# Optimization experiments

Hardware: AMD Instinct MI355X
Metric: run time of the kernel (lower is better)

The kernel has to match this reference:

```python
import jax, jax.numpy as jnp
import numpy as np

N_NODES = 100000
N_EDGES = 640000
D_IN = 128
HIDDEN = 256
OUT = 256
NUM_GRAPHS = 256


def setup_inputs() -> dict:
    key = jax.random.key(0)
    ks = jax.random.split(key, 8)
    x = jax.random.normal(ks[0], (N_NODES, D_IN), dtype=jnp.float32)
    edge_index = jax.random.randint(ks[1], (2, N_EDGES), 0, N_NODES, dtype=jnp.int64)
    batch = jnp.sort(jax.random.randint(ks[2], (N_NODES,), 0, NUM_GRAPHS, dtype=jnp.int64))
    s1 = 1.0 / np.sqrt(D_IN)
    s2 = 1.0 / np.sqrt(HIDDEN)
    W1_l = jax.random.normal(ks[3], (D_IN, HIDDEN), dtype=jnp.float32) * s1
    W1_r = jax.random.normal(ks[4], (D_IN, HIDDEN), dtype=jnp.float32) * s1
    b1 = jnp.zeros((HIDDEN,), dtype=jnp.float32)
    W2_l = jax.random.normal(ks[5], (HIDDEN, OUT), dtype=jnp.float32) * s2
    W2_r = jax.random.normal(ks[6], (HIDDEN, OUT), dtype=jnp.float32) * s2
    b2 = jnp.zeros((OUT,), dtype=jnp.float32)
    return {"x": x, "edge_index": edge_index, "batch": batch,
            "W1_l": W1_l, "b1": b1, "W1_r": W1_r,
            "W2_l": W2_l, "b2": b2, "W2_r": W2_r}


def _sage_conv(x, src, dst, W_l, b_l, W_r):
    # PyG SAGEConv, aggr='mean': lin_l(mean_{j in N(i)} x_j) + lin_r(x_i)
    n = x.shape[0]
    msgs = x[src]                                              # [E, d] gather
    agg = jax.ops.segment_sum(msgs, dst, num_segments=n)       # [N, d] scatter-add
    cnt = jax.ops.segment_sum(jnp.ones((src.shape[0],), x.dtype), dst, num_segments=n)
    mean = agg / jnp.maximum(cnt, 1.0)[:, None]
    return mean @ W_l + b_l + x @ W_r


def reference(x, edge_index, batch, W1_l, b1, W1_r, W2_l, b2, W2_r):
    src, dst = edge_index[0], edge_index[1]
    h = jax.nn.relu(_sage_conv(x, src, dst, W1_l, b1, W1_r))
    h = _sage_conv(h, src, dst, W2_l, b2, W2_r)
    # global_add_pool: segment sum over per-node graph ids
    return jax.ops.segment_sum(h, batch, num_segments=NUM_GRAPHS)  # [G, OUT]
```

## Files before the change

kernel.cpp:

```cpp
#include <hip/hip_runtime.h>

#define NN 100000
#define NE 640000
#define DIN 128
#define DH 256
#define DOUT 256
#define NG 256
#define NB1 ((NN + 255) / 256)

#define PECH 157
#define CPE (4 * PECH)
#define PEB ((NE + CPE - 1) / CPE)
#define GSP 8

#define PNB 1024
#define CHN2 ((NN + PNB - 1) / PNB)

#define BCH 4096
#define BNB ((NE + BCH - 1) / BCH)

#define ANW 8
#define AGW ((NN + ANW - 1) / ANW)
#define AGB ((AGW + 3) / 4)

typedef __bf16 bf16_t;
typedef __bf16 bf16x8 __attribute__((ext_vector_type(8)));
typedef float f32x4 __attribute__((ext_vector_type(4)));
typedef float f32v2 __attribute__((ext_vector_type(2)));

#if __has_builtin(__builtin_amdgcn_cvt_pk_fp8_f32) && __has_builtin(__builtin_amdgcn_cvt_pk_f32_fp8)
#define USE_HW_FP8 1
#else
#define USE_HW_FP8 0
#endif

#if !USE_HW_FP8
__device__ __forceinline__ unsigned f32_to_fp8_1(float f) {
  unsigned sg = (__float_as_uint(f) >> 31) << 7;
  float af = fabsf(f);
  unsigned body;
  if (af < 0.015625f) {
    body = (unsigned)(int)rintf(af * 512.0f);
  } else {
    unsigned bits = __float_as_uint(af);
    unsigned rb = bits + 0x7FFFFu + ((bits >> 20) & 1u);
    unsigned e = rb >> 23;
    body = ((e - 120u) << 3) | ((rb >> 20) & 7u);
  }
  return (sg | body) & 0xffu;
}
__device__ __forceinline__ float fp8_to_f32_1(unsigned b) {
  unsigned s = b >> 7, e = (b >> 3) & 15u, m = b & 7u;
  float v = (e == 0) ? (float)m * 0.001953125f
                     : __uint_as_float(((e + 120u) << 23) | (m << 20));
  return s ? -v : v;
}
#endif

__device__ __forceinline__ unsigned pack4_fp8(float v0, float v1, float v2, float v3) {
#if USE_HW_FP8
  int u = __builtin_amdgcn_cvt_pk_fp8_f32(v0, v1, 0, false);
  u = __builtin_amdgcn_cvt_pk_fp8_f32(v2, v3, u, true);
  return (unsigned)u;
#else
  return f32_to_fp8_1(v0) | (f32_to_fp8_1(v1) << 8) |
         (f32_to_fp8_1(v2) << 16) | (f32_to_fp8_1(v3) << 24);
#endif
}

__device__ __forceinline__ unsigned short pack2_fp8(float v0, float v1) {
#if USE_HW_FP8
  int u = __builtin_amdgcn_cvt_pk_fp8_f32(v0, v1, 0, false);
  return (unsigned short)(u & 0xffff);
#else
  return (unsigned short)(f32_to_fp8_1(v0) | (f32_to_fp8_1(v1) << 8));
#endif
}

__device__ __forceinline__ void unpack4_fp8(unsigned v, float* o) {
#if USE_HW_FP8
  f32v2 a = __builtin_amdgcn_cvt_pk_f32_fp8((int)v, false);
  f32v2 b = __builtin_amdgcn_cvt_pk_f32_fp8((int)v, true);
  o[0] = a[0]; o[1] = a[1]; o[2] = b[0]; o[3] = b[1];
#else
  o[0] = fp8_to_f32_1(v & 0xffu);         o[1] = fp8_to_f32_1((v >> 8) & 0xffu);
  o[2] = fp8_to_f32_1((v >> 16) & 0xffu); o[3] = fp8_to_f32_1(v >> 24);
#endif
}

__device__ __forceinline__ void unpack8_fp8(uint2 v, float* o) {
  unpack4_fp8(v.x, o);
  unpack4_fp8(v.y, o + 4);
}

__device__ __forceinline__ void unpack2_fp8(unsigned v, float* o) {
#if USE_HW_FP8
  f32v2 a = __builtin_amdgcn_cvt_pk_f32_fp8((int)v, false);
  o[0] = a[0]; o[1] = a[1];
#else
  o[0] = fp8_to_f32_1(v & 0xffu); o[1] = fp8_to_f32_1((v >> 8) & 0xffu);
#endif
}

__global__ void k_xcast(const float* __restrict__ x, unsigned char* __restrict__ xf8) {
  size_t i = ((size_t)blockIdx.x * 256 + threadIdx.x) * 8;
  if (i >= (size_t)NN * DIN) return;
  float4 a = *(const float4*)(x + i), b = *(const float4*)(x + i + 4);
  uint2 p;
  p.x = pack4_fp8(a.x, a.y, a.z, a.w);
  p.y = pack4_fp8(b.x, b.y, b.z, b.w);
  *(uint2*)(xf8 + i) = p;
}

__global__ void k_count(const int* __restrict__ dst, int* __restrict__ cnt) {
  int e = blockIdx.x * 256 + threadIdx.x;
  if (e < NE) atomicAdd(&cnt[dst[e]], 1);
}

__global__ void k_scan1(const int* __restrict__ cnt, int* __restrict__ rowptr,
                        int* __restrict__ part) {
  __shared__ int s[256];
  int t = threadIdx.x, i = blockIdx.x * 256 + t;
  int v = (i < NN) ? cnt[i] : 0;
  s[t] = v; __syncthreads();
#pragma unroll
  for (int off = 1; off < 256; off <<= 1) {
    int u = (t >= off) ? s[t - off] : 0;
    __syncthreads();
    s[t] += u;
    __syncthreads();
  }
  if (i < NN) rowptr[i] = s[t] - v;
  if (t == 255) part[blockIdx.x] = s[255];
}

__global__ void k_scan2(int* __restrict__ part) {
  __shared__ int s[512];
  int t = threadIdx.x;
  int v = (t < NB1) ? part[t] : 0;
  s[t] = v; __syncthreads();
#pragma unroll
  for (int off = 1; off < 512; off <<= 1) {
    int u = (t >= off) ? s[t - off] : 0;
    __syncthreads();
    s[t] += u;
    __syncthreads();
  }
  if (t < NB1) part[t] = s[t] - v;
}

__global__ void k_scan3(int* __restrict__ rowptr, const int* __restrict__ part) {
  int i = blockIdx.x * 256 + threadIdx.x;
  if (i < NN) rowptr[i] += part[i >> 8];
  if (i == 0) rowptr[NN] = NE;
}

__global__ void k_gstart2(const int* __restrict__ batch, const int* __restrict__ rowptr,
                          int* __restrict__ gstart, unsigned* __restrict__ wg) {
  int n = blockIdx.x * 256 + threadIdx.x;
  if (n >= NN) return;
  int b = batch[n];
  int prev = (n == 0) ? -1 : batch[n - 1];
  for (int g = prev + 1; g <= b; ++g) gstart[g] = n;
  if (n == NN - 1) {
    for (int g = b + 1; g <= NG; ++g) gstart[g] = NN;
  }
  int e0 = rowptr[n], e1 = rowptr[n + 1];
  unsigned val = ((unsigned)b << 16) | (unsigned)(e1 - e0);
  for (int e = e0; e < e1; ++e) wg[e] = val;
}

__global__ void k_bucket(const int* __restrict__ src, const int* __restrict__ dst,
                         const int* __restrict__ rowptr, int* __restrict__ fill,
                         int* __restrict__ col) {
  int cls = blockIdx.x & 7;
  int cb = blockIdx.x >> 3;
  int e0 = cb * BCH;
  int e1 = (e0 + BCH < NE) ? e0 + BCH : NE;
  for (int e = e0 + threadIdx.x; e < e1; e += 256) {
    int d = dst[e];
    if (((d >> 4) & 7) == cls) {
      int p = rowptr[d] + atomicAdd(&fill[d], 1);
      col[p] = src[e];
    }
  }
}

__global__ void k_agg1(const int* __restrict__ rowptr, const int* __restrict__ col,
                       const unsigned char* __restrict__ xf8, unsigned char* __restrict__ ag1f8) {
  int wid = (blockIdx.x * 256 + threadIdx.x) >> 6;
  int lane = threadIdx.x & 63;
  int n0 = wid * ANW;
  if (n0 >= NN) return;
  int n1 = n0 + ANW; if (n1 > NN) n1 = NN;
  int e = rowptr[n0];
  int eTot = rowptr[n1];
  int n = n0;
  int estart = e;
  int eend = rowptr[n0 + 1];
  float a0 = 0.f, a1 = 0.f;
#define AFLUSH()                                                              \
  do {                                                                        \
    float r = (eend > estart) ? __builtin_amdgcn_rcpf((float)(eend - estart)) \
                              : 0.f;                                          \
    *(unsigned short*)(ag1f8 + (size_t)n * DIN + lane * 2) =                  \
        pack2_fp8(a0 * r, a1 * r);                                            \
    a0 = 0.f; a1 = 0.f;                                                       \
    estart = eend; n++;                                                       \
    if (n < n1) eend = rowptr[n + 1];                                         \
  } while (0)
  while (e + 8 <= eTot) {
    unsigned v[8];
#pragma unroll
    for (int i = 0; i < 8; ++i) {
      int s = col[e + i];
      v[i] = *(const unsigned short*)(xf8 + (size_t)s * DIN + lane * 2);
    }
#pragma unroll
    for (int i = 0; i < 8; ++i) {
      while (e + i >= eend) AFLUSH();
      float o[2];
      unpack2_fp8(v[i], o);
      a0 += o[0]; a1 += o[1];
    }
    e += 8;
  }
  while (e < eTot) {
    int s = col[e];
    unsigned v = *(const unsigned short*)(xf8 + (size_t)s * DIN + lane * 2);
    while (e >= eend) AFLUSH();
    float o[2];
    unpack2_fp8(v, o);
    a0 += o[0]; a1 += o[1];
    ++e;
  }
  while (n < n1) AFLUSH();
#undef AFLUSH
}

__global__ void k_pack1(const float* __restrict__ Wl, const float* __restrict__ Wr,
                        bf16_t* __restrict__ Bp) {
  int t = blockIdx.x * 256 + threadIdx.x;
  if (t >= 8192) return;
  int lane = t & 63, nt = (t >> 6) & 15, kc = t >> 10;
  int n = nt * 16 + (lane & 15);
  int k0 = kc * 32 + (lane >> 4) * 8;
  bf16_t* o = Bp + ((size_t)(kc * 16 + nt) * 64 + lane) * 8;
  for (int j = 0; j < 8; ++j) {
    int k = k0 + j;
    float v = (k < 128) ? Wl[k * 256 + n] : Wr[(k - 128) * 256 + n];
    o[j] = (bf16_t)v;
  }
}

__launch_bounds__(256, 4)
__global__ void k_gemm1(const unsigned char* __restrict__ xf8,
                        const unsigned char* __restrict__ ag1f8,
                        const float* __restrict__ b1,
                        const bf16_t* __restrict__ Bp, unsigned char* __restrict__ hf8) {
  __shared__ unsigned char smem[64 * 512];
  int n0 = blockIdx.x * 64;
  int tid = threadIdx.x;
  {
    int row = tid >> 2, part = tid & 3;
    int node = n0 + row;
    unsigned sw = (row & 7) << 4;
    const uint2* ap = (const uint2*)(ag1f8 + (size_t)node * DIN);
    const uint2* xp = (const uint2*)(xf8 + (size_t)node * DIN);
#pragma unroll
    for (int i = 0; i < 4; ++i) {
      int mi = i * 4 + part;
      uint2 va = {0u, 0u}, vx = {0u, 0u};
      if (node < NN) { va = ap[mi]; vx = xp[mi]; }
      float oa[8], ox[8];
      unpack8_fp8(va, oa);
      unpack8_fp8(vx, ox);
      bf16x8 wa, wx;
#pragma unroll
      for (int j = 0; j < 8; ++j) { wa[j] = (bf16_t)oa[j]; wx[j] = (bf16_t)ox[j]; }
      *(bf16x8*)(smem + row * 512 + (((unsigned)(mi * 16)) ^ sw)) = wa;
      *(bf16x8*)(smem + row * 512 + ((unsigned)(256 + mi * 16) ^ sw)) = wx;
    }
  }
  __syncthreads();
  int wave = tid >> 6, lane = tid & 63, lhi = lane >> 4, llo = lane & 15;
  f32x4 acc[4][4] = {};
  const bf16x8* bptr = (const bf16x8*)Bp;
#pragma unroll
  for (int kc = 0; kc < 8; ++kc) {
    bf16x8 a[4], b[4];
#pragma unroll
    for (int mi = 0; mi < 4; ++mi) {
      int row = mi * 16 + llo;
      unsigned cb = ((unsigned)((kc * 32 + lhi * 8) * 2)) ^ ((row & 7) << 4);
      a[mi] = *(const bf16x8*)(smem + row * 512 + cb);
    }
#pragma unroll
    for (int ni = 0; ni < 4; ++ni)
      b[ni] = bptr[(kc * 16 + wave * 4 + ni) * 64 + lane];
#pragma unroll
    for (int mi = 0; mi < 4; ++mi)
#pragma unroll
      for (int ni = 0; ni < 4; ++ni)
        acc[mi][ni] = __builtin_amdgcn_mfma_f32_16x16x32_bf16(a[mi], b[ni], acc[mi][ni], 0, 0, 0);
  }
  float bias[4];
#pragma unroll
  for (int ni = 0; ni < 4; ++ni) bias[ni] = b1[wave * 64 + ni * 16 + llo];
#pragma unroll
  for (int mi = 0; mi < 4; ++mi)
#pragma unroll
    for (int j = 0; j < 4; ++j) {
      int node = n0 + mi * 16 + lhi * 4 + j;
      if (node < NN) {
        float v0 = fmaxf(acc[mi][0][j] + bias[0], 0.f);
        float v1 = fmaxf(acc[mi][1][j] + bias[1], 0.f);
        float v2 = fmaxf(acc[mi][2][j] + bias[2], 0.f);
        float v3 = fmaxf(acc[mi][3][j] + bias[3], 0.f);
        unsigned u = pack4_fp8(v0, v1, v2, v3);
        *(unsigned*)(hf8 + (size_t)node * 256 + wave * 64 + llo * 4) = u;
      }
    }
}

__global__ void k_poolE2(const int* __restrict__ col, const unsigned* __restrict__ wg,
                         const unsigned char* __restrict__ hf8, float* __restrict__ Y1) {
  __shared__ float gbuf[GSP][256];
  int tid = threadIdx.x;
  int c0 = blockIdx.x * CPE;
  int c1 = (c0 + CPE < NE) ? c0 + CPE : NE;
  if (c0 >= c1) return;
  int gmin = (int)(wg[c0] >> 16), gmax = (int)(wg[c1 - 1] >> 16);
  bool ldsok = (gmax - gmin) < GSP;
  for (int i = tid; i < GSP * 256; i += 256) (&gbuf[0][0])[i] = 0.f;
  __syncthreads();
  int wv = tid >> 6, lane = tid & 63;
  int e0 = __builtin_amdgcn_readfirstlane(c0 + wv * PECH);
  int e1 = e0 + PECH; if (e1 > c1) e1 = c1;
  int dmb = ((lane >> 4) << 6) | (lane & 15);
  float acc[4] = {0.f, 0.f, 0.f, 0.f};
  int curg = -1;
#define EFLUSH() do { if (curg >= 0) {                                        \
    if (ldsok) { float* gp = gbuf[curg - gmin];                               \
      atomicAdd(gp + (dmb | 0),  acc[0]); atomicAdd(gp + (dmb | 16), acc[1]); \
      atomicAdd(gp + (dmb | 32), acc[2]); atomicAdd(gp + (dmb | 48), acc[3]); \
    } else { float* yp = Y1 + (size_t)curg * 256;                             \
      unsafeAtomicAdd(yp + (dmb | 0),  acc[0]);                               \
      unsafeAtomicAdd(yp + (dmb | 16), acc[1]);                               \
      unsafeAtomicAdd(yp + (dmb | 32), acc[2]);                               \
      unsafeAtomicAdd(yp + (dmb | 48), acc[3]); }                             \
    acc[0] = acc[1] = acc[2] = acc[3] = 0.f; } } while (0)
  if (e0 < e1) {
    int e = e0;
    for (; e + 16 <= e1; e += 16) {
      unsigned wvv[16]; unsigned hv[16];
#pragma unroll
      for (int i = 0; i < 16; ++i) {
        int c = col[e + i];
        wvv[i] = wg[e + i];
        hv[i] = *(const unsigned*)(hf8 + (size_t)c * 256 + lane * 4);
      }
#pragma unroll
      for (int i = 0; i < 16; ++i) {
        int g = (int)(wvv[i] >> 16);
        if (g != curg) { EFLUSH(); curg = g; }
        float w = __builtin_amdgcn_rcpf((float)(wvv[i] & 0xffffu));
        float o[4]; unpack4_fp8(hv[i], o);
        acc[0] += w * o[0]; acc[1] += w * o[1];
        acc[2] += w * o[2]; acc[3] += w * o[3];
      }
    }
    for (; e < e1; ++e) {
      int c = col[e]; unsigned wv2 = wg[e];
      unsigned hvv = *(const unsigned*)(hf8 + (size_t)c * 256 + lane * 4);
      int g = (int)(wv2 >> 16);
      if (g != curg) { EFLUSH(); curg = g; }
      float w = __builtin_amdgcn_rcpf((float)(wv2 & 0xffffu));
      float o[4]; unpack4_fp8(hvv, o);
      acc[0] += w * o[0]; acc[1] += w * o[1];
      acc[2] += w * o[2]; acc[3] += w * o[3];
    }
    EFLUSH();
  }
#undef EFLUSH
  __syncthreads();
  if (ldsok) {
    int ng = gmax - gmin + 1;
    for (int gi = 0; gi < ng; ++gi)
      unsafeAtomicAdd(&Y1[(size_t)(gmin + gi) * 256 + tid], gbuf[gi][tid]);
  }
}

__global__ void k_poolN(const int* __restrict__ batch, const unsigned char* __restrict__ hf8,
                        float* __restrict__ Y2) {
  __shared__ float gbuf[GSP][256];
  int tid = threadIdx.x;
  int n0 = blockIdx.x * CHN2;
  int n1 = (n0 + CHN2 < NN) ? n0 + CHN2 : NN;
  if (n0 >= n1) return;
  int gmin = batch[n0], gmax = batch[n1 - 1];
  bool ldsok = (gmax - gmin) < GSP;
  for (int i = tid; i < GSP * 256; i += 256) (&gbuf[0][0])[i] = 0.f;
  __syncthreads();
  int wv = tid >> 6, lane = tid & 63;
  const int per = (CHN2 + 3) >> 2;
  int a0 = n0 + wv * per;
  int a1 = a0 + per; if (a1 > n1) a1 = n1;
  int dmb = ((lane >> 4) << 6) | (lane & 15);
  float acc[4] = {0.f, 0.f, 0.f, 0.f};
  int curg = -1;
#define NFLUSH() do { if (curg >= 0) {                                        \
    if (ldsok) { float* gp = gbuf[curg - gmin];                               \
      atomicAdd(gp + (dmb | 0),  acc[0]); atomicAdd(gp + (dmb | 16), acc[1]); \
      atomicAdd(gp + (dmb | 32), acc[2]); atomicAdd(gp + (dmb | 48), acc[3]); \
    } else { float* yp = Y2 + (size_t)curg * 256;                             \
      unsafeAtomicAdd(yp + (dmb | 0),  acc[0]);                               \
      unsafeAtomicAdd(yp + (dmb | 16), acc[1]);                               \
      unsafeAtomicAdd(yp + (dmb | 32), acc[2]);                               \
      unsafeAtomicAdd(yp + (dmb | 48), acc[3]); }                             \
    acc[0] = acc[1] = acc[2] = acc[3] = 0.f; } } while (0)
  for (int n = a0; n < a1; ++n) {
    int g = batch[n];
    if (g != curg) { NFLUSH(); curg = g; }
    unsigned v = *(const unsigned*)(hf8 + (size_t)n * 256 + lane * 4);
    float o[4]; unpack4_fp8(v, o);
    acc[0] += o[0]; acc[1] += o[1]; acc[2] += o[2]; acc[3] += o[3];
  }
  NFLUSH();
#undef NFLUSH
  __syncthreads();
  if (ldsok) {
    int ng = gmax - gmin + 1;
    for (int gi = 0; gi < ng; ++gi)
      unsafeAtomicAdd(&Y2[(size_t)(gmin + gi) * 256 + tid], gbuf[gi][tid]);
  }
}

__global__ void k_out2(const float* __restrict__ Y1, const float* __restrict__ Y2,
                       const float* __restrict__ W2l, const float* __restrict__ W2r,
                       const float* __restrict__ b2, const int* __restrict__ gstart,
                       float* __restrict__ out) {
  __shared__ float ys[128];
  int g = blockIdx.x, ks = blockIdx.y, t = threadIdx.x;
  const float* Ysrc = (ks < 2) ? Y1 : Y2;
  const float* Wsrc = (ks < 2) ? W2l : W2r;
  int kbase = (ks & 1) * 128;
  if (t < 128) ys[t] = Ysrc[(size_t)g * 256 + kbase + t];
  __syncthreads();
  float s = 0.f;
  const float* wp = Wsrc + (size_t)kbase * 256 + t;
#pragma unroll 8
  for (int k = 0; k < 128; ++k) s += ys[k] * wp[(size_t)k * 256];
  if (ks == 0) {
    float cntf = (float)(gstart[g + 1] - gstart[g]);
    s += b2[t] * cntf;
  }
  unsafeAtomicAdd(&out[(size_t)g * 256 + t], s);
}

extern "C" void kernel_launch(void* const* d_in, const int* in_sizes, int n_in,
                              void* d_out, int out_size, void* d_ws, size_t ws_size,
                              hipStream_t stream) {
  const float* x   = (const float*)d_in[0];
  const int*   ei  = (const int*)d_in[1];
  const int*   bat = (const int*)d_in[2];
  const float* W1l = (const float*)d_in[3];
  const float* b1  = (const float*)d_in[4];
  const float* W1r = (const float*)d_in[5];
  const float* W2l = (const float*)d_in[6];
  const float* b2  = (const float*)d_in[7];
  const float* W2r = (const float*)d_in[8];
  const int* src = ei;
  const int* dst = ei + NE;

  char* ws = (char*)d_ws;
  size_t off = 0;
  int* cnt     = (int*)(ws + off); off += ((size_t)NN * 4 + 255) & ~(size_t)255;
  int* rowptr  = (int*)(ws + off); off += ((size_t)(NN + 1) * 4 + 255) & ~(size_t)255;
  int* part    = (int*)(ws + off); off += 512 * 4;
  int* fill    = (int*)(ws + off); off += ((size_t)NN * 4 + 255) & ~(size_t)255;
  int* gstart  = (int*)(ws + off); off += ((size_t)(NG + 1) * 4 + 255) & ~(size_t)255;
  int* col     = (int*)(ws + off); off += (size_t)NE * 4;
  unsigned* wg = (unsigned*)(ws + off); off += (size_t)NE * 4;
  bf16_t* Bp1  = (bf16_t*)(ws + off); off += (size_t)256 * 256 * 2;
  float* Y1    = (float*)(ws + off); off += (size_t)NG * 256 * 4;
  float* Y2    = (float*)(ws + off); off += (size_t)NG * 256 * 4;
  unsigned char* xf8 = (unsigned char*)(ws + off); off += (size_t)NN * DIN;
  unsigned char* ag1f8 = (unsigned char*)(ws + off); off += (size_t)NN * DIN;
  unsigned char* hf8 = (unsigned char*)(ws + off); off += (size_t)NN * DH;

  hipMemsetAsync(cnt, 0, (size_t)NN * 4, stream);
  hipMemsetAsync(fill, 0, (size_t)NN * 4, stream);
  hipMemsetAsync(Y1, 0, (size_t)NG * 256 * 4 * 2, stream);
  hipMemsetAsync(d_out, 0, (size_t)out_size * 4, stream);
  k_xcast<<<NN * DIN / 8 / 256, 256, 0, stream>>>(x, xf8);
  k_pack1<<<32, 256, 0, stream>>>(W1l, W1r, Bp1);
  k_count<<<(NE + 255) / 256, 256, 0, stream>>>(dst, cnt);
  k_scan1<<<NB1, 256, 0, stream>>>(cnt, rowptr, part);
  k_scan2<<<1, 512, 0, stream>>>(part);
  k_scan3<<<NB1, 256, 0, stream>>>(rowptr, part);
  k_gstart2<<<NB1, 256, 0, stream>>>(bat, rowptr, gstart, wg);
  k_bucket<<<BNB * 8, 256, 0, stream>>>(src, dst, rowptr, fill, col);
  k_agg1<<<AGB, 256, 0, stream>>>(rowptr, col, xf8, ag1f8);
  k_gemm1<<<(NN + 63) / 64, 256, 0, stream>>>(xf8, ag1f8, b1, Bp1, hf8);
  k_poolE2<<<PEB, 256, 0, stream>>>(col, wg, hf8, Y1);
  k_poolN<<<PNB, 256, 0, stream>>>(bat, hf8, Y2);
  k_out2<<<dim3(NG, 4), 256, 0, stream>>>(Y1, Y2, W2l, W2r, b2, gstart, (float*)d_out);
}
```

Before: 202.1 us.

## Fuse neighbor mean aggregation into GEMM1 and merge small setup and pool kernels

The first-layer neighbor aggregation now runs inside the GEMM kernel. Each wave gathers fp8 neighbor rows for 16 nodes and writes the bf16 means straight into shared memory, so the ag1f8 intermediate is no longer written to and read back from global memory. The x cast, edge count and weight pack kernels are merged into one launch, the scan fixup is folded into the gstart/wg kernel, and the two pooling kernels become one grid with block ranges. This removes several launches and a global round trip, but the irregular gather now sits inside the GEMM block, which may stall the MFMA work and lower its occupancy.

```diff
diff --git a/kernel.cpp b/kernel.cpp
--- a/kernel.cpp
+++ b/kernel.cpp
@@ -19,12 +19,12 @@
 #define BCH 4096
 #define BNB ((NE + BCH - 1) / BCH)
 
-#define ANW 8
-#define AGW ((NN + ANW - 1) / ANW)
-#define AGB ((AGW + 3) / 4)
+#define XCB (NN * DIN / 8 / 256)
+#define CTB ((NE + 255) / 256)
 
 typedef __bf16 bf16_t;
 typedef __bf16 bf16x8 __attribute__((ext_vector_type(8)));
+typedef __bf16 bf16x2 __attribute__((ext_vector_type(2)));
 typedef float f32x4 __attribute__((ext_vector_type(4)));
 typedef float f32v2 __attribute__((ext_vector_type(2)));
 
@@ -68,15 +68,6 @@
 #endif
 }
 
-__device__ __forceinline__ unsigned short pack2_fp8(float v0, float v1) {
-#if USE_HW_FP8
-  int u = __builtin_amdgcn_cvt_pk_fp8_f32(v0, v1, 0, false);
-  return (unsigned short)(u & 0xffff);
-#else
-  return (unsigned short)(f32_to_fp8_1(v0) | (f32_to_fp8_1(v1) << 8));
-#endif
-}
-
 __device__ __forceinline__ void unpack4_fp8(unsigned v, float* o) {
 #if USE_HW_FP8
   f32v2 a = __builtin_amdgcn_cvt_pk_f32_fp8((int)v, false);
@@ -88,11 +79,6 @@
 #endif
 }
 
-__device__ __forceinline__ void unpack8_fp8(uint2 v, float* o) {
-  unpack4_fp8(v.x, o);
-  unpack4_fp8(v.y, o + 4);
-}
-
 __device__ __forceinline__ void unpack2_fp8(unsigned v, float* o) {
 #if USE_HW_FP8
   f32v2 a = __builtin_amdgcn_cvt_pk_f32_fp8((int)v, false);
@@ -102,22 +88,38 @@
 #endif
 }
 
-__global__ void k_xcast(const float* __restrict__ x, unsigned char* __restrict__ xf8) {
-  size_t i = ((size_t)blockIdx.x * 256 + threadIdx.x) * 8;
-  if (i >= (size_t)NN * DIN) return;
-  float4 a = *(const float4*)(x + i), b = *(const float4*)(x + i + 4);
-  uint2 p;
-  p.x = pack4_fp8(a.x, a.y, a.z, a.w);
-  p.y = pack4_fp8(b.x, b.y, b.z, b.w);
-  *(uint2*)(xf8 + i) = p;
-}
-
-__global__ void k_count(const int* __restrict__ dst, int* __restrict__ cnt) {
-  int e = blockIdx.x * 256 + threadIdx.x;
-  if (e < NE) atomicAdd(&cnt[dst[e]], 1);
-}
-
-__global__ void k_scan1(const int* __restrict__ cnt, int* __restrict__ rowptr,
+__global__ void k_pre(const float* __restrict__ x, const int* __restrict__ dst,
+                      const float* __restrict__ Wl, const float* __restrict__ Wr,
+                      unsigned char* __restrict__ xf8, int* __restrict__ cnt,
+                      bf16_t* __restrict__ Bp) {
+  int b = blockIdx.x;
+  if (b < XCB) {
+    size_t i = ((size_t)b * 256 + threadIdx.x) * 8;
+    float4 a = *(const float4*)(x + i), c = *(const float4*)(x + i + 4);
+    uint2 p;
+    p.x = pack4_fp8(a.x, a.y, a.z, a.w);
+    p.y = pack4_fp8(c.x, c.y, c.z, c.w);
+    *(uint2*)(xf8 + i) = p;
+  } else if (b < XCB + CTB) {
+    int e = (b - XCB) * 256 + threadIdx.x;
+    if (e < NE) atomicAdd(&cnt[dst[e]], 1);
+  } else {
+    int t = (b - XCB - CTB) * 256 + threadIdx.x;
+    if (t < 8192) {
+      int lane = t & 63, nt = (t >> 6) & 15, kc = t >> 10;
+      int n = nt * 16 + (lane & 15);
+      int k0 = kc * 32 + (lane >> 4) * 8;
+      bf16_t* o = Bp + ((size_t)(kc * 16 + nt) * 64 + lane) * 8;
+      for (int j = 0; j < 8; ++j) {
+        int k = k0 + j;
+        float v = (k < 128) ? Wl[k * 256 + n] : Wr[(k - 128) * 256 + n];
+        o[j] = (bf16_t)v;
+      }
+    }
+  }
+}
+
+__global__ void k_scan1(const int* __restrict__ cnt, int* __restrict__ rpl,
                         int* __restrict__ part) {
   __shared__ int s[256];
   int t = threadIdx.x, i = blockIdx.x * 256 + t;
@@ -130,7 +132,7 @@
     s[t] += u;
     __syncthreads();
   }
-  if (i < NN) rowptr[i] = s[t] - v;
+  if (i < NN) rpl[i] = s[t] - v;
   if (t == 255) part[blockIdx.x] = s[255];
 }
 
@@ -149,25 +151,23 @@
   if (t < NB1) part[t] = s[t] - v;
 }
 
-__global__ void k_scan3(int* __restrict__ rowptr, const int* __restrict__ part) {
-  int i = blockIdx.x * 256 + threadIdx.x;
-  if (i < NN) rowptr[i] += part[i >> 8];
-  if (i == 0) rowptr[NN] = NE;
-}
-
-__global__ void k_gstart2(const int* __restrict__ batch, const int* __restrict__ rowptr,
-                          int* __restrict__ gstart, unsigned* __restrict__ wg) {
+__global__ void k_finish(const int* __restrict__ rpl, const int* __restrict__ part,
+                         const int* __restrict__ batch, int* __restrict__ rowptr,
+                         int* __restrict__ gstart, unsigned* __restrict__ wg) {
   int n = blockIdx.x * 256 + threadIdx.x;
   if (n >= NN) return;
+  int r0 = rpl[n] + part[n >> 8];
+  int r1 = (n + 1 < NN) ? (rpl[n + 1] + part[(n + 1) >> 8]) : NE;
+  rowptr[n] = r0;
+  if (n == 0) rowptr[NN] = NE;
   int b = batch[n];
   int prev = (n == 0) ? -1 : batch[n - 1];
   for (int g = prev + 1; g <= b; ++g) gstart[g] = n;
   if (n == NN - 1) {
     for (int g = b + 1; g <= NG; ++g) gstart[g] = NN;
   }
-  int e0 = rowptr[n], e1 = rowptr[n + 1];
-  unsigned val = ((unsigned)b << 16) | (unsigned)(e1 - e0);
-  for (int e = e0; e < e1; ++e) wg[e] = val;
+  unsigned val = ((unsigned)b << 16) | (unsigned)(r1 - r0);
+  for (int e = r0; e < r1; ++e) wg[e] = val;
 }
 
 __global__ void k_bucket(const int* __restrict__ src, const int* __restrict__ dst,
@@ -186,104 +186,77 @@
   }
 }
 
-__global__ void k_agg1(const int* __restrict__ rowptr, const int* __restrict__ col,
-                       const unsigned char* __restrict__ xf8, unsigned char* __restrict__ ag1f8) {
-  int wid = (blockIdx.x * 256 + threadIdx.x) >> 6;
-  int lane = threadIdx.x & 63;
-  int n0 = wid * ANW;
-  if (n0 >= NN) return;
-  int n1 = n0 + ANW; if (n1 > NN) n1 = NN;
-  int e = rowptr[n0];
-  int eTot = rowptr[n1];
-  int n = n0;
-  int estart = e;
-  int eend = rowptr[n0 + 1];
-  float a0 = 0.f, a1 = 0.f;
-#define AFLUSH()                                                              \
-  do {                                                                        \
-    float r = (eend > estart) ? __builtin_amdgcn_rcpf((float)(eend - estart)) \
-                              : 0.f;                                          \
-    *(unsigned short*)(ag1f8 + (size_t)n * DIN + lane * 2) =                  \
-        pack2_fp8(a0 * r, a1 * r);                                            \
-    a0 = 0.f; a1 = 0.f;                                                       \
-    estart = eend; n++;                                                       \
-    if (n < n1) eend = rowptr[n + 1];                                         \
-  } while (0)
-  while (e + 8 <= eTot) {
-    unsigned v[8];
-#pragma unroll
-    for (int i = 0; i < 8; ++i) {
-      int s = col[e + i];
-      v[i] = *(const unsigned short*)(xf8 + (size_t)s * DIN + lane * 2);
-    }
-#pragma unroll
-    for (int i = 0; i < 8; ++i) {
-      while (e + i >= eend) AFLUSH();
-      float o[2];
-      unpack2_fp8(v[i], o);
-      a0 += o[0]; a1 += o[1];
-    }
-    e += 8;
-  }
-  while (e < eTot) {
-    int s = col[e];
-    unsigned v = *(const unsigned short*)(xf8 + (size_t)s * DIN + lane * 2);
-    while (e >= eend) AFLUSH();
-    float o[2];
-    unpack2_fp8(v, o);
-    a0 += o[0]; a1 += o[1];
-    ++e;
-  }
-  while (n < n1) AFLUSH();
-#undef AFLUSH
-}
-
-__global__ void k_pack1(const float* __restrict__ Wl, const float* __restrict__ Wr,
-                        bf16_t* __restrict__ Bp) {
-  int t = blockIdx.x * 256 + threadIdx.x;
-  if (t >= 8192) return;
-  int lane = t & 63, nt = (t >> 6) & 15, kc = t >> 10;
-  int n = nt * 16 + (lane & 15);
-  int k0 = kc * 32 + (lane >> 4) * 8;
-  bf16_t* o = Bp + ((size_t)(kc * 16 + nt) * 64 + lane) * 8;
-  for (int j = 0; j < 8; ++j) {
-    int k = k0 + j;
-    float v = (k < 128) ? Wl[k * 256 + n] : Wr[(k - 128) * 256 + n];
-    o[j] = (bf16_t)v;
-  }
-}
-
 __launch_bounds__(256, 4)
 __global__ void k_gemm1(const unsigned char* __restrict__ xf8,
-                        const unsigned char* __restrict__ ag1f8,
+                        const int* __restrict__ rowptr, const int* __restrict__ col,
                         const float* __restrict__ b1,
                         const bf16_t* __restrict__ Bp, unsigned char* __restrict__ hf8) {
   __shared__ unsigned char smem[64 * 512];
   int n0 = blockIdx.x * 64;
   int tid = threadIdx.x;
+  int wave = tid >> 6, lane = tid & 63;
   {
-    int row = tid >> 2, part = tid & 3;
-    int node = n0 + row;
-    unsigned sw = (row & 7) << 4;
-    const uint2* ap = (const uint2*)(ag1f8 + (size_t)node * DIN);
-    const uint2* xp = (const uint2*)(xf8 + (size_t)node * DIN);
-#pragma unroll
-    for (int i = 0; i < 4; ++i) {
-      int mi = i * 4 + part;
-      uint2 va = {0u, 0u}, vx = {0u, 0u};
-      if (node < NN) { va = ap[mi]; vx = xp[mi]; }
-      float oa[8], ox[8];
-      unpack8_fp8(va, oa);
-      unpack8_fp8(vx, ox);
-      bf16x8 wa, wx;
-#pragma unroll
-      for (int j = 0; j < 8; ++j) { wa[j] = (bf16_t)oa[j]; wx[j] = (bf16_t)ox[j]; }
-      *(bf16x8*)(smem + row * 512 + (((unsigned)(mi * 16)) ^ sw)) = wa;
-      *(bf16x8*)(smem + row * 512 + ((unsigned)(256 + mi * 16) ^ sw)) = wx;
+    int base = __builtin_amdgcn_readfirstlane(n0 + wave * 16);
+    int nb1 = base + 16; if (nb1 > NN) nb1 = NN;
+    if (base < NN) {
+      int e = rowptr[base];
+      int eTot = rowptr[nb1];
+      int n = base;
+      int estart = e;
+      int eend = rowptr[n + 1];
+      float a0 = 0.f, a1 = 0.f;
+#define GFLUSH()                                                               \
+      do {                                                                     \
+        float r = (eend > estart)                                              \
+                    ? __builtin_amdgcn_rcpf((float)(eend - estart)) : 0.f;     \
+        int row = n - n0;                                                      \
+        unsigned sw = (row & 7) << 4;                                          \
+        bf16x2 mv; mv[0] = (bf16_t)(a0 * r); mv[1] = (bf16_t)(a1 * r);         \
+        *(bf16x2*)(smem + row * 512 + (((unsigned)(lane * 4)) ^ sw)) = mv;     \
+        a0 = 0.f; a1 = 0.f;                                                    \
+        estart = eend; ++n;                                                    \
+        if (n < nb1) eend = rowptr[n + 1];                                     \
+      } while (0)
+      while (e + 8 <= eTot) {
+        unsigned v[8];
+#pragma unroll
+        for (int i = 0; i < 8; ++i) {
+          int s = col[e + i];
+          v[i] = *(const unsigned short*)(xf8 + (size_t)s * DIN + lane * 2);
+        }
+#pragma unroll
+        for (int i = 0; i < 8; ++i) {
+          while (e + i >= eend) GFLUSH();
+          float o[2]; unpack2_fp8(v[i], o);
+          a0 += o[0]; a1 += o[1];
+        }
+        e += 8;
+      }
+      while (e < eTot) {
+        int s = col[e];
+        unsigned v = *(const unsigned short*)(xf8 + (size_t)s * DIN + lane * 2);
+        while (e >= eend) GFLUSH();
+        float o[2]; unpack2_fp8(v, o);
+        a0 += o[0]; a1 += o[1];
+        ++e;
+      }
+      while (n < nb1) GFLUSH();
+#undef GFLUSH
+    }
+#pragma unroll
+    for (int i = 0; i < 16; ++i) {
+      int node = base + i;
+      int row = wave * 16 + i;
+      unsigned sw = (row & 7) << 4;
+      unsigned v = 0;
+      if (node < NN) v = *(const unsigned short*)(xf8 + (size_t)node * DIN + lane * 2);
+      float o[2]; unpack2_fp8(v, o);
+      bf16x2 xv; xv[0] = (bf16_t)o[0]; xv[1] = (bf16_t)o[1];
+      *(bf16x2*)(smem + row * 512 + ((unsigned)(256 + lane * 4) ^ sw)) = xv;
     }
   }
   __syncthreads();
-  int wave = tid >> 6, lane = tid & 63, lhi = lane >> 4, llo = lane & 15;
+  int lhi = lane >> 4, llo = lane & 15;
   f32x4 acc[4][4] = {};
   const bf16x8* bptr = (const bf16x8*)Bp;
 #pragma unroll
@@ -323,23 +296,25 @@
     }
 }
 
-__global__ void k_poolE2(const int* __restrict__ col, const unsigned* __restrict__ wg,
-                         const unsigned char* __restrict__ hf8, float* __restrict__ Y1) {
+__global__ void k_pool(const int* __restrict__ col, const unsigned* __restrict__ wg,
+                       const int* __restrict__ batch, const unsigned char* __restrict__ hf8,
+                       float* __restrict__ Y1, float* __restrict__ Y2) {
   __shared__ float gbuf[GSP][256];
   int tid = threadIdx.x;
-  int c0 = blockIdx.x * CPE;
-  int c1 = (c0 + CPE < NE) ? c0 + CPE : NE;
-  if (c0 >= c1) return;
-  int gmin = (int)(wg[c0] >> 16), gmax = (int)(wg[c1 - 1] >> 16);
-  bool ldsok = (gmax - gmin) < GSP;
-  for (int i = tid; i < GSP * 256; i += 256) (&gbuf[0][0])[i] = 0.f;
-  __syncthreads();
   int wv = tid >> 6, lane = tid & 63;
-  int e0 = __builtin_amdgcn_readfirstlane(c0 + wv * PECH);
-  int e1 = e0 + PECH; if (e1 > c1) e1 = c1;
   int dmb = ((lane >> 4) << 6) | (lane & 15);
   float acc[4] = {0.f, 0.f, 0.f, 0.f};
   int curg = -1;
+  if (blockIdx.x < PEB) {
+    int c0 = blockIdx.x * CPE;
+    int c1 = (c0 + CPE < NE) ? c0 + CPE : NE;
+    if (c0 >= c1) return;
+    int gmin = (int)(wg[c0] >> 16), gmax = (int)(wg[c1 - 1] >> 16);
+    bool ldsok = (gmax - gmin) < GSP;
+    for (int i = tid; i < GSP * 256; i += 256) (&gbuf[0][0])[i] = 0.f;
+    __syncthreads();
+    int e0 = __builtin_amdgcn_readfirstlane(c0 + wv * PECH);
+    int e1 = e0 + PECH; if (e1 > c1) e1 = c1;
 #define EFLUSH() do { if (curg >= 0) {                                        \
     if (ldsok) { float* gp = gbuf[curg - gmin];                               \
       atomicAdd(gp + (dmb | 0),  acc[0]); atomicAdd(gp + (dmb | 16), acc[1]); \
@@ -350,65 +325,57 @@
       unsafeAtomicAdd(yp + (dmb | 32), acc[2]);                               \
       unsafeAtomicAdd(yp + (dmb | 48), acc[3]); }                             \
     acc[0] = acc[1] = acc[2] = acc[3] = 0.f; } } while (0)
-  if (e0 < e1) {
-    int e = e0;
-    for (; e + 16 <= e1; e += 16) {
-      unsigned wvv[16]; unsigned hv[16];
-#pragma unroll
-      for (int i = 0; i < 16; ++i) {
-        int c = col[e + i];
-        wvv[i] = wg[e + i];
-        hv[i] = *(const unsigned*)(hf8 + (size_t)c * 256 + lane * 4);
-      }
-#pragma unroll
-      for (int i = 0; i < 16; ++i) {
-        int g = (int)(wvv[i] >> 16);
+    if (e0 < e1) {
+      int e = e0;
+      for (; e + 16 <= e1; e += 16) {
+        unsigned wvv[16]; unsigned hv[16];
+#pragma unroll
+        for (int i = 0; i < 16; ++i) {
+          int c = col[e + i];
+          wvv[i] = wg[e + i];
+          hv[i] = *(const unsigned*)(hf8 + (size_t)c * 256 + lane * 4);
+        }
+#pragma unroll
+        for (int i = 0; i < 16; ++i) {
+          int g = (int)(wvv[i] >> 16);
+          if (g != curg) { EFLUSH(); curg = g; }
+          float w = __builtin_amdgcn_rcpf((float)(wvv[i] & 0xffffu));
+          float o[4]; unpack4_fp8(hv[i], o);
+          acc[0] += w * o[0]; acc[1] += w * o[1];
+          acc[2] += w * o[2]; acc[3] += w * o[3];
+        }
+      }
+      for (; e < e1; ++e) {
+        int c = col[e]; unsigned wv2 = wg[e];
+        unsigned hvv = *(const unsigned*)(hf8 + (size_t)c * 256 + lane * 4);
+        int g = (int)(wv2 >> 16);
         if (g != curg) { EFLUSH(); curg = g; }
-        float w = __builtin_amdgcn_rcpf((float)(wvv[i] & 0xffffu));
-        float o[4]; unpack4_fp8(hv[i], o);
+        float w = __builtin_amdgcn_rcpf((float)(wv2 & 0xffffu));
+        float o[4]; unpack4_fp8(hvv, o);
         acc[0] += w * o[0]; acc[1] += w * o[1];
         acc[2] += w * o[2]; acc[3] += w * o[3];
       }
-    }
-    for (; e < e1; ++e) {
-      int c = col[e]; unsigned wv2 = wg[e];
-      unsigned hvv = *(const unsigned*)(hf8 + (size_t)c * 256 + lane * 4);
-      int g = (int)(wv2 >> 16);
-      if (g != curg) { EFLUSH(); curg = g; }
-      float w = __builtin_amdgcn_rcpf((float)(wv2 & 0xffffu));
-      float o[4]; unpack4_fp8(hvv, o);
-      acc[0] += w * o[0]; acc[1] += w * o[1];
-      acc[2] += w * o[2]; acc[3] += w * o[3];
-    }
-    EFLUSH();
-  }
+      EFLUSH();
+    }
 #undef EFLUSH
-  __syncthreads();
-  if (ldsok) {
-    int ng = gmax - gmin + 1;
-    for (int gi = 0; gi < ng; ++gi)
-      unsafeAtomicAdd(&Y1[(size_t)(gmin + gi) * 256 + tid], gbuf[gi][tid]);
-  }
-}
-
-__global__ void k_poolN(const int* __restrict__ batch, const unsigned char* __restrict__ hf8,
-                        float* __restrict__ Y2) {
-  __shared__ float gbuf[GSP][256];
-  int tid = threadIdx.x;
-  int n0 = blockIdx.x * CHN2;
-  int n1 = (n0 + CHN2 < NN) ? n0 + CHN2 : NN;
-  if (n0 >= n1) return;
-  int gmin = batch[n0], gmax = batch[n1 - 1];
-  bool ldsok = (gmax - gmin) < GSP;
-  for (int i = tid; i < GSP * 256; i += 256) (&gbuf[0][0])[i] = 0.f;
-  __syncthreads();
-  int wv = tid >> 6, lane = tid & 63;
-  const int per = (CHN2 + 3) >> 2;
-  int a0 = n0 + wv * per;
-  int a1 = a0 + per; if (a1 > n1) a1 = n1;
-  int dmb = ((lane >> 4) << 6) | (lane & 15);
-  float acc[4] = {0.f, 0.f, 0.f, 0.f};
-  int curg = -1;
+    __syncthreads();
+    if (ldsok) {
+      int ng = gmax - gmin + 1;
+      for (int gi = 0; gi < ng; ++gi)
+        unsafeAtomicAdd(&Y1[(size_t)(gmin + gi) * 256 + tid], gbuf[gi][tid]);
+    }
+  } else {
+    int nb = blockIdx.x - PEB;
+    int n0 = nb * CHN2;
+    int n1 = (n0 + CHN2 < NN) ? n0 + CHN2 : NN;
+    if (n0 >= n1) return;
+    int gmin = batch[n0], gmax = batch[n1 - 1];
+    bool ldsok = (gmax - gmin) < GSP;
+    for (int i = tid; i < GSP * 256; i += 256) (&gbuf[0][0])[i] = 0.f;
+    __syncthreads();
+    const int per = (CHN2 + 3) >> 2;
+    int a0 = n0 + wv * per;
+    int a1 = a0 + per; if (a1 > n1) a1 = n1;
 #define NFLUSH() do { if (curg >= 0) {                                        \
     if (ldsok) { float* gp = gbuf[curg - gmin];                               \
       atomicAdd(gp + (dmb | 0),  acc[0]); atomicAdd(gp + (dmb | 16), acc[1]); \
@@ -419,20 +386,21 @@
       unsafeAtomicAdd(yp + (dmb | 32), acc[2]);                               \
       unsafeAtomicAdd(yp + (dmb | 48), acc[3]); }                             \
     acc[0] = acc[1] = acc[2] = acc[3] = 0.f; } } while (0)
-  for (int n = a0; n < a1; ++n) {
-    int g = batch[n];
-    if (g != curg) { NFLUSH(); curg = g; }
-    unsigned v = *(const unsigned*)(hf8 + (size_t)n * 256 + lane * 4);
-    float o[4]; unpack4_fp8(v, o);
-    acc[0] += o[0]; acc[1] += o[1]; acc[2] += o[2]; acc[3] += o[3];
-  }
-  NFLUSH();
+    for (int n = a0; n < a1; ++n) {
+      int g = batch[n];
+      if (g != curg) { NFLUSH(); curg = g; }
+      unsigned v = *(const unsigned*)(hf8 + (size_t)n * 256 + lane * 4);
+      float o[4]; unpack4_fp8(v, o);
+      acc[0] += o[0]; acc[1] += o[1]; acc[2] += o[2]; acc[3] += o[3];
+    }
+    NFLUSH();
 #undef NFLUSH
-  __syncthreads();
-  if (ldsok) {
-    int ng = gmax - gmin + 1;
-    for (int gi = 0; gi < ng; ++gi)
-      unsafeAtomicAdd(&Y2[(size_t)(gmin + gi) * 256 + tid], gbuf[gi][tid]);
+    __syncthreads();
+    if (ldsok) {
+      int ng = gmax - gmin + 1;
+      for (int gi = 0; gi < ng; ++gi)
+        unsafeAtomicAdd(&Y2[(size_t)(gmin + gi) * 256 + tid], gbuf[gi][tid]);
+    }
   }
 }
 
@@ -476,6 +444,7 @@
   char* ws = (char*)d_ws;
   size_t off = 0;
   int* cnt     = (int*)(ws + off); off += ((size_t)NN * 4 + 255) & ~(size_t)255;
+  int* rpl     = (int*)(ws + off); off += ((size_t)(NN + 1) * 4 + 255) & ~(size_t)255;
   int* rowptr  = (int*)(ws + off); off += ((size_t)(NN + 1) * 4 + 255) & ~(size_t)255;
   int* part    = (int*)(ws + off); off += 512 * 4;
   int* fill    = (int*)(ws + off); off += ((size_t)NN * 4 + 255) & ~(size_t)255;
@@ -486,24 +455,18 @@
   float* Y1    = (float*)(ws + off); off += (size_t)NG * 256 * 4;
   float* Y2    = (float*)(ws + off); off += (size_t)NG * 256 * 4;
   unsigned char* xf8 = (unsigned char*)(ws + off); off += (size_t)NN * DIN;
-  unsigned char* ag1f8 = (unsigned char*)(ws + off); off += (size_t)NN * DIN;
   unsigned char* hf8 = (unsigned char*)(ws + off); off += (size_t)NN * DH;
 
   hipMemsetAsync(cnt, 0, (size_t)NN * 4, stream);
   hipMemsetAsync(fill, 0, (size_t)NN * 4, stream);
   hipMemsetAsync(Y1, 0, (size_t)NG * 256 * 4 * 2, stream);
   hipMemsetAsync(d_out, 0, (size_t)out_size * 4, stream);
-  k_xcast<<<NN * DIN / 8 / 256, 256, 0, stream>>>(x, xf8);
-  k_pack1<<<32, 256, 0, stream>>>(W1l, W1r, Bp1);
-  k_count<<<(NE + 255) / 256, 256, 0, stream>>>(dst, cnt);
-  k_scan1<<<NB1, 256, 0, stream>>>(cnt, rowptr, part);
+  k_pre<<<XCB + CTB + 32, 256, 0, stream>>>(x, dst, W1l, W1r, xf8, cnt, Bp1);
+  k_scan1<<<NB1, 256, 0, stream>>>(cnt, rpl, part);
   k_scan2<<<1, 512, 0, stream>>>(part);
-  k_scan3<<<NB1, 256, 0, stream>>>(rowptr, part);
-  k_gstart2<<<NB1, 256, 0, stream>>>(bat, rowptr, gstart, wg);
+  k_finish<<<NB1, 256, 0, stream>>>(rpl, part, bat, rowptr, gstart, wg);
   k_bucket<<<BNB * 8, 256, 0, stream>>>(src, dst, rowptr, fill, col);
-  k_agg1<<<AGB, 256, 0, stream>>>(rowptr, col, xf8, ag1f8);
-  k_gemm1<<<(NN + 63) / 64, 256, 0, stream>>>(xf8, ag1f8, b1, Bp1, hf8);
-  k_poolE2<<<PEB, 256, 0, stream>>>(col, wg, hf8, Y1);
-  k_poolN<<<PNB, 256, 0, stream>>>(bat, hf8, Y2);
+  k_gemm1<<<(NN + 63) / 64, 256, 0, stream>>>(xf8, rowptr, col, b1, Bp1, hf8);
+  k_pool<<<PEB + PNB, 256, 0, stream>>>(col, wg, bat, hf8, Y1, Y2);
   k_out2<<<dim3(NG, 4), 256, 0, stream>>>(Y1, Y2, W2l, W2r, b2, gstart, (float*)d_out);
 }
```

After: 185.4 us. -8.3%, faster.
